# Kernel optimization log

Hardware: AMD Instinct MI355X
Metric: run time of the kernel (lower is better)

## Reference

```python
import jax, jax.numpy as jnp
import numpy as np

NUM_EMB = 512
EMB_DIM = 64
COMMIT = 0.25
DECAY = 0.99
EPS = 1e-05


def setup_inputs() -> dict:
    key = jax.random.key(0)
    k1, k2, k3 = jax.random.split(key, 3)
    inputs = jax.random.normal(k1, (EMB_DIM, 16, 8192), dtype=jnp.float32)  # [D, B, T]
    embedding = jax.random.normal(k2, (NUM_EMB, EMB_DIM), dtype=jnp.float32)
    ema_w = jax.random.normal(k3, (NUM_EMB, EMB_DIM), dtype=jnp.float32)
    ema_cluster_size = jnp.zeros((NUM_EMB,), dtype=jnp.float32)
    return {"inputs": inputs, "embedding": embedding, "ema_w": ema_w,
            "ema_cluster_size": ema_cluster_size}


def reference(inputs, embedding, ema_w, ema_cluster_size):
    # [D, B, T] -> [B, T, D]
    x = jnp.transpose(inputs, (1, 2, 0))
    in_shape = x.shape
    flat = x.reshape(-1, EMB_DIM)  # [N, D]

    # Squared L2 distances to every codebook entry: [N, K]
    distances = (jnp.sum(flat ** 2, axis=1, keepdims=True)
                 + jnp.sum(embedding ** 2, axis=1)
                 - 2.0 * flat @ embedding.T)
    idx = jnp.argmin(distances, axis=1)                       # [N]
    encodings = jax.nn.one_hot(idx, NUM_EMB, dtype=jnp.float32)  # [N, K]

    # EMA codebook update (training mode). torch wraps results in nn.Parameter,
    # which detaches them, so we stop_gradient the updated embedding.
    cluster = ema_cluster_size * DECAY + (1.0 - DECAY) * jnp.sum(encodings, axis=0)
    n = jnp.sum(cluster)
    cluster = (cluster + EPS) / (n + NUM_EMB * EPS) * n
    dw = jax.ops.segment_sum(flat, idx, num_segments=NUM_EMB)  # == encodings.T @ flat
    new_ema_w = ema_w * DECAY + (1.0 - DECAY) * dw
    new_emb = jax.lax.stop_gradient(new_ema_w / cluster[:, None])  # [K, D]

    # Quantize via gather (equivalent to encodings @ new_emb)
    quantized = new_emb[idx].reshape(in_shape)  # [B, T, D]

    e_latent_loss = jnp.mean((jax.lax.stop_gradient(quantized) - x) ** 2)
    loss = COMMIT * e_latent_loss

    # Straight-through estimator
    quantized_st = x + jax.lax.stop_gradient(quantized - x)

    avg_probs = jnp.mean(encodings, axis=0)
    perplexity = jnp.exp(-jnp.sum(avg_probs * jnp.log(avg_probs + 1e-10)))

    return (loss, jnp.transpose(quantized_st, (2, 0, 1)), perplexity, encodings, distances)
```

## Files before the change

### kernel.cpp

```cpp
#include <hip/hip_runtime.h>

#define NTOT 131072
#define KCB  512
#define DIM  64

__device__ __forceinline__ float wave_sum(float v) {
#pragma unroll
  for (int off = 32; off; off >>= 1) v += __shfl_xor(v, off, 64);
  return v;
}

__global__ __launch_bounds__(512, 2) void k_dist(
    const float* __restrict__ x_g,
    const float* __restrict__ emb_g,
    float* __restrict__ dist_out,
    float* __restrict__ enc_out,
    int* __restrict__ idx_out,
    unsigned* __restrict__ cnt_g,
    float* __restrict__ dw_g)
{
  __shared__ __align__(16) float embt[DIM][KCB];
  __shared__ __align__(16) float embsq[KCB];
  __shared__ float xtile[DIM][65];
  __shared__ float xq[64];
  __shared__ unsigned lcnt[KCB];

  const int t = threadIdx.x;
  const int lane = t & 63;
  const int w = t >> 6;

  lcnt[t] = 0u;

  {
    const float* er = emb_g + t * DIM;
    float sq = 0.f;
#pragma unroll
    for (int d0 = 0; d0 < DIM; d0 += 4) {
      const float4 e = *reinterpret_cast<const float4*>(er + d0);
      embt[d0 + 0][t] = -2.f * e.x;
      embt[d0 + 1][t] = -2.f * e.y;
      embt[d0 + 2][t] = -2.f * e.z;
      embt[d0 + 3][t] = -2.f * e.w;
      sq = fmaf(e.x, e.x, sq); sq = fmaf(e.y, e.y, sq);
      sq = fmaf(e.z, e.z, sq); sq = fmaf(e.w, e.w, sq);
    }
    embsq[t] = sq;
  }

  const int rows_pb = NTOT / 256;
  const int nb = blockIdx.x * rows_pb;

  for (int tt = 0; tt < rows_pb; tt += 64) {
    const int n0 = nb + tt;
    __syncthreads();
#pragma unroll
    for (int dd = 0; dd < 8; ++dd) {
      const int d = w * 8 + dd;
      xtile[d][lane] = x_g[(size_t)d * NTOT + (n0 + lane)];
    }
    __syncthreads();
    if (w == 0) {
      float s = 0.f;
#pragma unroll
      for (int d = 0; d < DIM; ++d) { const float v = xtile[d][lane]; s = fmaf(v, v, s); }
      xq[lane] = s;
    }
    __syncthreads();

    const int rb = w * 8;
    float xr[8];
#pragma unroll
    for (int r = 0; r < 8; ++r) xr[r] = xtile[lane][rb + r];

    const float4 eb0 = *reinterpret_cast<const float4*>(&embsq[4 * lane]);
    const float4 eb1 = *reinterpret_cast<const float4*>(&embsq[256 + 4 * lane]);
    float acc[8][8];
#pragma unroll
    for (int r = 0; r < 8; ++r) {
      acc[r][0] = eb0.x; acc[r][1] = eb0.y; acc[r][2] = eb0.z; acc[r][3] = eb0.w;
      acc[r][4] = eb1.x; acc[r][5] = eb1.y; acc[r][6] = eb1.z; acc[r][7] = eb1.w;
    }

#pragma unroll 4
    for (int d = 0; d < DIM; ++d) {
      const float4 e0 = *reinterpret_cast<const float4*>(&embt[d][4 * lane]);
      const float4 e1 = *reinterpret_cast<const float4*>(&embt[d][256 + 4 * lane]);
#pragma unroll
      for (int r = 0; r < 8; ++r) {
        const float s = __uint_as_float(
            __builtin_amdgcn_readlane(__float_as_uint(xr[r]), d));
        acc[r][0] = fmaf(s, e0.x, acc[r][0]);
        acc[r][1] = fmaf(s, e0.y, acc[r][1]);
        acc[r][2] = fmaf(s, e0.z, acc[r][2]);
        acc[r][3] = fmaf(s, e0.w, acc[r][3]);
        acc[r][4] = fmaf(s, e1.x, acc[r][4]);
        acc[r][5] = fmaf(s, e1.y, acc[r][5]);
        acc[r][6] = fmaf(s, e1.z, acc[r][6]);
        acc[r][7] = fmaf(s, e1.w, acc[r][7]);
      }
    }

#pragma unroll
    for (int r = 0; r < 8; ++r) {
      const int nr = n0 + rb + r;
      const float xs = xq[rb + r];
      float dv[8];
#pragma unroll
      for (int j = 0; j < 8; ++j) dv[j] = acc[r][j] + xs;

      unsigned long long best = ~0ull;
#pragma unroll
      for (int j = 0; j < 8; ++j) {
        const unsigned kk = (j < 4) ? (unsigned)(4 * lane + j)
                                    : (unsigned)(256 + 4 * lane + (j - 4));
        const unsigned long long pk =
            ((unsigned long long)__float_as_uint(dv[j]) << 32) | kk;
        best = pk < best ? pk : best;
      }
#pragma unroll
      for (int off = 32; off; off >>= 1) {
        const unsigned long long o = __shfl_xor(best, off, 64);
        best = o < best ? o : best;
      }
      const int kmin = (int)(best & 0xFFFFFFFFull);

      float* dp = dist_out + (size_t)nr * KCB + 4 * lane;
      float2 p;
      p.x = dv[0]; p.y = dv[1]; *reinterpret_cast<float2*>(dp) = p;
      p.x = dv[2]; p.y = dv[3]; *reinterpret_cast<float2*>(dp + 2) = p;
      p.x = dv[4]; p.y = dv[5]; *reinterpret_cast<float2*>(dp + 256) = p;
      p.x = dv[6]; p.y = dv[7]; *reinterpret_cast<float2*>(dp + 258) = p;

      float* ep = enc_out + (size_t)nr * KCB + 4 * lane;
      const int k0 = 4 * lane;
      float2 z;
      z.x = (kmin == k0)           ? 1.f : 0.f;
      z.y = (kmin == k0 + 1)       ? 1.f : 0.f;
      *reinterpret_cast<float2*>(ep) = z;
      z.x = (kmin == k0 + 2)       ? 1.f : 0.f;
      z.y = (kmin == k0 + 3)       ? 1.f : 0.f;
      *reinterpret_cast<float2*>(ep + 2) = z;
      z.x = (kmin == 256 + k0)     ? 1.f : 0.f;
      z.y = (kmin == 256 + k0 + 1) ? 1.f : 0.f;
      *reinterpret_cast<float2*>(ep + 256) = z;
      z.x = (kmin == 256 + k0 + 2) ? 1.f : 0.f;
      z.y = (kmin == 256 + k0 + 3) ? 1.f : 0.f;
      *reinterpret_cast<float2*>(ep + 258) = z;

      if (lane == 0) {
        idx_out[nr] = kmin;
        atomicAdd(&lcnt[kmin], 1u);
      }
      unsafeAtomicAdd(dw_g + ((size_t)kmin << 6) + lane, xr[r]);
    }
  }

  __syncthreads();
  if (lcnt[t]) atomicAdd(&cnt_g[t], lcnt[t]);
}

__global__ __launch_bounds__(512, 1) void k_final(
    const float* __restrict__ ema_w, const float* __restrict__ ema_cs,
    const unsigned* __restrict__ cnt, const float* __restrict__ dw,
    float* __restrict__ nemb, float* __restrict__ out)
{
  __shared__ float red[8];
  __shared__ float bc;
  const int t = threadIdx.x;
  const int lane = t & 63, w = t >> 6;

  const float c = (float)cnt[t];
  const float craw = ema_cs[t] * 0.99f + 0.01f * c;

  float s = wave_sum(craw);
  if (lane == 0) red[w] = s;
  __syncthreads();
  if (t == 0) {
    float a = 0.f;
#pragma unroll
    for (int i = 0; i < 8; ++i) a += red[i];
    bc = a;
  }
  __syncthreads();
  const float n = bc;
  const float clus = (craw + 1e-5f) / (n + 512.f * 1e-5f) * n;

  const float4* wr = reinterpret_cast<const float4*>(ema_w + t * 64);
  const float4* dr = reinterpret_cast<const float4*>(dw + t * 64);
  float4* nr = reinterpret_cast<float4*>(nemb + t * 64);
#pragma unroll
  for (int q = 0; q < 16; ++q) {
    const float4 wv = wr[q], dv = dr[q];
    float4 o;
    o.x = (wv.x * 0.99f + 0.01f * dv.x) / clus;
    o.y = (wv.y * 0.99f + 0.01f * dv.y) / clus;
    o.z = (wv.z * 0.99f + 0.01f * dv.z) / clus;
    o.w = (wv.w * 0.99f + 0.01f * dv.w) / clus;
    nr[q] = o;
  }

  const float p = c * (1.f / 131072.f);
  const float term = p * logf(p + 1e-10f);
  float s2 = wave_sum(term);
  if (lane == 0) red[w] = s2;
  __syncthreads();
  if (t == 0) {
    float a = 0.f;
#pragma unroll
    for (int i = 0; i < 8; ++i) a += red[i];
    out[8388609] = expf(-a);
  }
}

__global__ __launch_bounds__(256, 4) void k_quant(
    const float* __restrict__ x_g, const int* __restrict__ idx_g,
    const float* __restrict__ nemb, float* __restrict__ out)
{
  float lsum = 0.f;
  const int stride = gridDim.x * 256;
  for (int i = blockIdx.x * 256 + threadIdx.x; i < (DIM * NTOT / 4); i += stride) {
    const int d = i >> 15;
    const int n4 = i & ((NTOT / 4) - 1);
    const float4 xv = *reinterpret_cast<const float4*>(x_g + ((size_t)d << 17) + 4 * n4);
    const int4 id = *reinterpret_cast<const int4*>(idx_g + 4 * n4);
    const float q0 = nemb[(id.x << 6) + d];
    const float q1 = nemb[(id.y << 6) + d];
    const float q2 = nemb[(id.z << 6) + d];
    const float q3 = nemb[(id.w << 6) + d];
    const float e0 = q0 - xv.x, e1 = q1 - xv.y, e2 = q2 - xv.z, e3 = q3 - xv.w;
    float* op = out + 1 + ((size_t)d << 17) + 4 * n4;
    op[0] = xv.x + e0;
    op[1] = xv.y + e1;
    op[2] = xv.z + e2;
    op[3] = xv.w + e3;
    lsum += e0 * e0 + e1 * e1 + e2 * e2 + e3 * e3;
  }
  lsum = wave_sum(lsum);
  __shared__ float wsum[4];
  const int lane = threadIdx.x & 63, w = threadIdx.x >> 6;
  if (lane == 0) wsum[w] = lsum;
  __syncthreads();
  if (threadIdx.x == 0)
    unsafeAtomicAdd(out, (wsum[0] + wsum[1] + wsum[2] + wsum[3]) * (0.25f / 8388608.f));
}

extern "C" void kernel_launch(void* const* d_in, const int* in_sizes, int n_in,
                              void* d_out, int out_size, void* d_ws, size_t ws_size,
                              hipStream_t stream) {
  const float* x      = (const float*)d_in[0];
  const float* emb    = (const float*)d_in[1];
  const float* ema_w  = (const float*)d_in[2];
  const float* ema_cs = (const float*)d_in[3];
  float* out = (float*)d_out;

  float* enc_out  = out + 8388610;
  float* dist_out = out + 75497474;

  char* ws = (char*)d_ws;
  float*    dw   = (float*)ws;
  unsigned* cnt  = (unsigned*)(ws + 131072);
  float*    nemb = (float*)(ws + 133120);
  int*      idx  = (int*)(ws + 264192);

  hipMemsetAsync(d_ws, 0, 133120, stream);
  hipMemsetAsync(d_out, 0, sizeof(float), stream);

  k_dist<<<256, 512, 0, stream>>>(x, emb, dist_out, enc_out, idx, cnt, dw);
  k_final<<<1, 512, 0, stream>>>(ema_w, ema_cs, cnt, dw, nemb, out);
  k_quant<<<2048, 256, 0, stream>>>(x, idx, nemb, out);
}
```

Baseline: 246.3 us.

## Privatize dw/count atomics per block and rework distance tile to per-wave 16 rows

After: 310.6 us. +26.1%, slower.

```diff
diff --git a/kernel.cpp b/kernel.cpp
--- a/kernel.cpp
+++ b/kernel.cpp
@@ -16,24 +16,20 @@
     float* __restrict__ dist_out,
     float* __restrict__ enc_out,
     int* __restrict__ idx_out,
-    unsigned* __restrict__ cnt_g,
-    float* __restrict__ dw_g)
+    unsigned* __restrict__ cnt_p,
+    float* __restrict__ dw_p,
+    int npart)
 {
   __shared__ __align__(16) float embt[DIM][KCB];
-  __shared__ __align__(16) float embsq[KCB];
-  __shared__ float xtile[DIM][65];
-  __shared__ float xq[64];
-  __shared__ unsigned lcnt[KCB];
+  __shared__ __align__(16) float xls[8][16][DIM];
 
   const int t = threadIdx.x;
   const int lane = t & 63;
   const int w = t >> 6;
-
-  lcnt[t] = 0u;
+  const int part = blockIdx.x & (npart - 1);
 
   {
     const float* er = emb_g + t * DIM;
-    float sq = 0.f;
 #pragma unroll
     for (int d0 = 0; d0 < DIM; d0 += 4) {
       const float4 e = *reinterpret_cast<const float4*>(er + d0);
@@ -41,69 +37,106 @@
       embt[d0 + 1][t] = -2.f * e.y;
       embt[d0 + 2][t] = -2.f * e.z;
       embt[d0 + 3][t] = -2.f * e.w;
-      sq = fmaf(e.x, e.x, sq); sq = fmaf(e.y, e.y, sq);
-      sq = fmaf(e.z, e.z, sq); sq = fmaf(e.w, e.w, sq);
     }
-    embsq[t] = sq;
-  }
-
-  const int rows_pb = NTOT / 256;
-  const int nb = blockIdx.x * rows_pb;
-
-  for (int tt = 0; tt < rows_pb; tt += 64) {
-    const int n0 = nb + tt;
-    __syncthreads();
-#pragma unroll
-    for (int dd = 0; dd < 8; ++dd) {
-      const int d = w * 8 + dd;
-      xtile[d][lane] = x_g[(size_t)d * NTOT + (n0 + lane)];
+  }
+  __syncthreads();
+
+  float ebr[8] = {0.f, 0.f, 0.f, 0.f, 0.f, 0.f, 0.f, 0.f};
+  for (int d = 0; d < DIM; ++d) {
+    const float4 a = *reinterpret_cast<const float4*>(&embt[d][4 * lane]);
+    const float4 b = *reinterpret_cast<const float4*>(&embt[d][256 + 4 * lane]);
+    ebr[0] = fmaf(a.x, a.x, ebr[0]); ebr[1] = fmaf(a.y, a.y, ebr[1]);
+    ebr[2] = fmaf(a.z, a.z, ebr[2]); ebr[3] = fmaf(a.w, a.w, ebr[3]);
+    ebr[4] = fmaf(b.x, b.x, ebr[4]); ebr[5] = fmaf(b.y, b.y, ebr[5]);
+    ebr[6] = fmaf(b.z, b.z, ebr[6]); ebr[7] = fmaf(b.w, b.w, ebr[7]);
+  }
+#pragma unroll
+  for (int j = 0; j < 8; ++j) ebr[j] *= 0.25f;
+
+  const int nb = blockIdx.x * 512;
+  const int r_own = lane & 15;
+  const int dgrp  = lane >> 4;
+
+  for (int tt = 0; tt < 4; ++tt) {
+    const int n0w = nb + tt * 128 + w * 16;
+
+    asm volatile("" ::: "memory");
+
+    float xv[16];
+#pragma unroll
+    for (int j = 0; j < 16; ++j)
+      xv[j] = x_g[(size_t)(4 * j + dgrp) * NTOT + n0w + r_own];
+#pragma unroll
+    for (int j = 0; j < 16; ++j)
+      xls[w][r_own][4 * j + dgrp] = xv[j];
+
+    asm volatile("" ::: "memory");
+
+    float ps = 0.f;
+#pragma unroll
+    for (int j = 0; j < 16; ++j) ps = fmaf(xv[j], xv[j], ps);
+    ps += __shfl_xor(ps, 16, 64);
+    ps += __shfl_xor(ps, 32, 64);
+
+    float acc[16][8];
+#pragma unroll
+    for (int r = 0; r < 16; ++r)
+#pragma unroll
+      for (int j = 0; j < 8; ++j) acc[r][j] = ebr[j];
+
+    for (int q = 0; q < 16; ++q) {
+      float4 e0[4], e1[4];
+#pragma unroll
+      for (int dq = 0; dq < 4; ++dq) {
+        e0[dq] = *reinterpret_cast<const float4*>(&embt[4 * q + dq][4 * lane]);
+        e1[dq] = *reinterpret_cast<const float4*>(&embt[4 * q + dq][256 + 4 * lane]);
+      }
+#pragma unroll
+      for (int r = 0; r < 16; ++r) {
+        const float4 xb = *reinterpret_cast<const float4*>(&xls[w][r][4 * q]);
+        acc[r][0] = fmaf(xb.x, e0[0].x, acc[r][0]);
+        acc[r][1] = fmaf(xb.x, e0[0].y, acc[r][1]);
+        acc[r][2] = fmaf(xb.x, e0[0].z, acc[r][2]);
+        acc[r][3] = fmaf(xb.x, e0[0].w, acc[r][3]);
+        acc[r][4] = fmaf(xb.x, e1[0].x, acc[r][4]);
+        acc[r][5] = fmaf(xb.x, e1[0].y, acc[r][5]);
+        acc[r][6] = fmaf(xb.x, e1[0].z, acc[r][6]);
+        acc[r][7] = fmaf(xb.x, e1[0].w, acc[r][7]);
+
+        acc[r][0] = fmaf(xb.y, e0[1].x, acc[r][0]);
+        acc[r][1] = fmaf(xb.y, e0[1].y, acc[r][1]);
+        acc[r][2] = fmaf(xb.y, e0[1].z, acc[r][2]);
+        acc[r][3] = fmaf(xb.y, e0[1].w, acc[r][3]);
+        acc[r][4] = fmaf(xb.y, e1[1].x, acc[r][4]);
+        acc[r][5] = fmaf(xb.y, e1[1].y, acc[r][5]);
+        acc[r][6] = fmaf(xb.y, e1[1].z, acc[r][6]);
+        acc[r][7] = fmaf(xb.y, e1[1].w, acc[r][7]);
+
+        acc[r][0] = fmaf(xb.z, e0[2].x, acc[r][0]);
+        acc[r][1] = fmaf(xb.z, e0[2].y, acc[r][1]);
+        acc[r][2] = fmaf(xb.z, e0[2].z, acc[r][2]);
+        acc[r][3] = fmaf(xb.z, e0[2].w, acc[r][3]);
+        acc[r][4] = fmaf(xb.z, e1[2].x, acc[r][4]);
+        acc[r][5] = fmaf(xb.z, e1[2].y, acc[r][5]);
+        acc[r][6] = fmaf(xb.z, e1[2].z, acc[r][6]);
+        acc[r][7] = fmaf(xb.z, e1[2].w, acc[r][7]);
+
+        acc[r][0] = fmaf(xb.w, e0[3].x, acc[r][0]);
+        acc[r][1] = fmaf(xb.w, e0[3].y, acc[r][1]);
+        acc[r][2] = fmaf(xb.w, e0[3].z, acc[r][2]);
+        acc[r][3] = fmaf(xb.w, e0[3].w, acc[r][3]);
+        acc[r][4] = fmaf(xb.w, e1[3].x, acc[r][4]);
+        acc[r][5] = fmaf(xb.w, e1[3].y, acc[r][5]);
+        acc[r][6] = fmaf(xb.w, e1[3].z, acc[r][6]);
+        acc[r][7] = fmaf(xb.w, e1[3].w, acc[r][7]);
+      }
     }
-    __syncthreads();
-    if (w == 0) {
-      float s = 0.f;
-#pragma unroll
-      for (int d = 0; d < DIM; ++d) { const float v = xtile[d][lane]; s = fmaf(v, v, s); }
-      xq[lane] = s;
-    }
-    __syncthreads();
-
-    const int rb = w * 8;
-    float xr[8];
-#pragma unroll
-    for (int r = 0; r < 8; ++r) xr[r] = xtile[lane][rb + r];
-
-    const float4 eb0 = *reinterpret_cast<const float4*>(&embsq[4 * lane]);
-    const float4 eb1 = *reinterpret_cast<const float4*>(&embsq[256 + 4 * lane]);
-    float acc[8][8];
-#pragma unroll
-    for (int r = 0; r < 8; ++r) {
-      acc[r][0] = eb0.x; acc[r][1] = eb0.y; acc[r][2] = eb0.z; acc[r][3] = eb0.w;
-      acc[r][4] = eb1.x; acc[r][5] = eb1.y; acc[r][6] = eb1.z; acc[r][7] = eb1.w;
-    }
-
-#pragma unroll 4
-    for (int d = 0; d < DIM; ++d) {
-      const float4 e0 = *reinterpret_cast<const float4*>(&embt[d][4 * lane]);
-      const float4 e1 = *reinterpret_cast<const float4*>(&embt[d][256 + 4 * lane]);
-#pragma unroll
-      for (int r = 0; r < 8; ++r) {
-        const float s = __uint_as_float(
-            __builtin_amdgcn_readlane(__float_as_uint(xr[r]), d));
-        acc[r][0] = fmaf(s, e0.x, acc[r][0]);
-        acc[r][1] = fmaf(s, e0.y, acc[r][1]);
-        acc[r][2] = fmaf(s, e0.z, acc[r][2]);
-        acc[r][3] = fmaf(s, e0.w, acc[r][3]);
-        acc[r][4] = fmaf(s, e1.x, acc[r][4]);
-        acc[r][5] = fmaf(s, e1.y, acc[r][5]);
-        acc[r][6] = fmaf(s, e1.z, acc[r][6]);
-        acc[r][7] = fmaf(s, e1.w, acc[r][7]);
-      }
-    }
-
-#pragma unroll
-    for (int r = 0; r < 8; ++r) {
-      const int nr = n0 + rb + r;
-      const float xs = xq[rb + r];
+
+#pragma unroll
+    for (int r = 0; r < 16; ++r) {
+      const int nr = n0w + r;
+      const float xs = __uint_as_float(
+          __builtin_amdgcn_readlane(__float_as_uint(ps), r));
       float dv[8];
 #pragma unroll
       for (int j = 0; j < 8; ++j) dv[j] = acc[r][j] + xs;
@@ -149,14 +182,29 @@
 
       if (lane == 0) {
         idx_out[nr] = kmin;
-        atomicAdd(&lcnt[kmin], 1u);
-      }
-      unsafeAtomicAdd(dw_g + ((size_t)kmin << 6) + lane, xr[r]);
+        atomicAdd(cnt_p + (size_t)part * KCB + kmin, 1u);
+      }
+      const float xrow = xls[w][r][lane];
+      unsafeAtomicAdd(dw_p + (size_t)part * (KCB * DIM) + (kmin << 6) + lane, xrow);
     }
   }
-
-  __syncthreads();
-  if (lcnt[t]) atomicAdd(&cnt_g[t], lcnt[t]);
+}
+
+__global__ __launch_bounds__(256, 8) void k_red(
+    const float* __restrict__ dw_p, const unsigned* __restrict__ cnt_p,
+    float* __restrict__ dwsum, unsigned* __restrict__ cnt, int npart)
+{
+  const int t = blockIdx.x * 256 + threadIdx.x;
+  float s = 0.f;
+#pragma unroll 4
+  for (int p = 0; p < npart; ++p) s += dw_p[(size_t)p * (KCB * DIM) + t];
+  dwsum[t] = s;
+  if (t < KCB) {
+    unsigned c = 0u;
+#pragma unroll 4
+    for (int p = 0; p < npart; ++p) c += cnt_p[(size_t)p * KCB + t];
+    cnt[t] = c;
+  }
 }
 
 __global__ __launch_bounds__(512, 1) void k_final(
@@ -257,15 +305,22 @@
   float* dist_out = out + 75497474;
 
   char* ws = (char*)d_ws;
-  float*    dw   = (float*)ws;
-  unsigned* cnt  = (unsigned*)(ws + 131072);
-  float*    nemb = (float*)(ws + 133120);
-  int*      idx  = (int*)(ws + 264192);
-
-  hipMemsetAsync(d_ws, 0, 133120, stream);
+  float*    dwsum = (float*)ws;
+  unsigned* cnt   = (unsigned*)(ws + 131072);
+  float*    nemb  = (float*)(ws + 133120);
+  int*      idx   = (int*)(ws + 264192);
+
+  int npart = 256;
+  while (npart > 1 &&
+         (size_t)788480 + (size_t)npart * 133120 > ws_size) npart >>= 1;
+  unsigned* cnt_p = (unsigned*)(ws + 788480);
+  float*    dw_p  = (float*)(ws + 788480 + (size_t)npart * 2048);
+
+  hipMemsetAsync(ws + 788480, 0, (size_t)npart * 133120, stream);
   hipMemsetAsync(d_out, 0, sizeof(float), stream);
 
-  k_dist<<<256, 512, 0, stream>>>(x, emb, dist_out, enc_out, idx, cnt, dw);
-  k_final<<<1, 512, 0, stream>>>(ema_w, ema_cs, cnt, dw, nemb, out);
+  k_dist<<<256, 512, 0, stream>>>(x, emb, dist_out, enc_out, idx, cnt_p, dw_p, npart);
+  k_red<<<128, 256, 0, stream>>>(dw_p, cnt_p, dwsum, cnt, npart);
+  k_final<<<1, 512, 0, stream>>>(ema_w, ema_cs, cnt, dwsum, nemb, out);
   k_quant<<<2048, 256, 0, stream>>>(x, idx, nemb, out);
 }
```

## Make x tile staging per-wave and drop block barriers in distance loop

Applied to the files above, without the earlier changes.

Result: faster. 239.0 us (-3.0%).

```diff
diff --git a/kernel.cpp b/kernel.cpp
--- a/kernel.cpp
+++ b/kernel.cpp
@@ -20,9 +20,7 @@
     float* __restrict__ dw_g)
 {
   __shared__ __align__(16) float embt[DIM][KCB];
-  __shared__ __align__(16) float embsq[KCB];
-  __shared__ float xtile[DIM][65];
-  __shared__ float xq[64];
+  __shared__ __align__(16) float xls[8][8][65];
   __shared__ unsigned lcnt[KCB];
 
   const int t = threadIdx.x;
@@ -33,7 +31,6 @@
 
   {
     const float* er = emb_g + t * DIM;
-    float sq = 0.f;
 #pragma unroll
     for (int d0 = 0; d0 < DIM; d0 += 4) {
       const float4 e = *reinterpret_cast<const float4*>(er + d0);
@@ -41,45 +38,57 @@
       embt[d0 + 1][t] = -2.f * e.y;
       embt[d0 + 2][t] = -2.f * e.z;
       embt[d0 + 3][t] = -2.f * e.w;
-      sq = fmaf(e.x, e.x, sq); sq = fmaf(e.y, e.y, sq);
-      sq = fmaf(e.z, e.z, sq); sq = fmaf(e.w, e.w, sq);
     }
-    embsq[t] = sq;
-  }
-
-  const int rows_pb = NTOT / 256;
-  const int nb = blockIdx.x * rows_pb;
-
-  for (int tt = 0; tt < rows_pb; tt += 64) {
-    const int n0 = nb + tt;
-    __syncthreads();
-#pragma unroll
-    for (int dd = 0; dd < 8; ++dd) {
-      const int d = w * 8 + dd;
-      xtile[d][lane] = x_g[(size_t)d * NTOT + (n0 + lane)];
-    }
-    __syncthreads();
-    if (w == 0) {
-      float s = 0.f;
-#pragma unroll
-      for (int d = 0; d < DIM; ++d) { const float v = xtile[d][lane]; s = fmaf(v, v, s); }
-      xq[lane] = s;
-    }
-    __syncthreads();
-
-    const int rb = w * 8;
+  }
+  __syncthreads();
+
+  float ebr[8] = {0.f, 0.f, 0.f, 0.f, 0.f, 0.f, 0.f, 0.f};
+  for (int d = 0; d < DIM; ++d) {
+    const float4 a = *reinterpret_cast<const float4*>(&embt[d][4 * lane]);
+    const float4 b = *reinterpret_cast<const float4*>(&embt[d][256 + 4 * lane]);
+    ebr[0] = fmaf(a.x, a.x, ebr[0]); ebr[1] = fmaf(a.y, a.y, ebr[1]);
+    ebr[2] = fmaf(a.z, a.z, ebr[2]); ebr[3] = fmaf(a.w, a.w, ebr[3]);
+    ebr[4] = fmaf(b.x, b.x, ebr[4]); ebr[5] = fmaf(b.y, b.y, ebr[5]);
+    ebr[6] = fmaf(b.z, b.z, ebr[6]); ebr[7] = fmaf(b.w, b.w, ebr[7]);
+  }
+#pragma unroll
+  for (int j = 0; j < 8; ++j) ebr[j] *= 0.25f;
+
+  const int nb = blockIdx.x * 512;
+  const int r_own = lane & 7;
+  const int dgc   = lane >> 3;
+
+  for (int tt = 0; tt < 8; ++tt) {
+    const int n0w = nb + tt * 64 + w * 8;
+
+    asm volatile("" ::: "memory");
+
+    float xv[8];
+#pragma unroll
+    for (int j = 0; j < 8; ++j)
+      xv[j] = x_g[(size_t)(dgc * 8 + j) * NTOT + n0w + r_own];
+#pragma unroll
+    for (int j = 0; j < 8; ++j)
+      xls[w][r_own][dgc * 8 + j] = xv[j];
+
+    asm volatile("" ::: "memory");
+
+    float ps = 0.f;
+#pragma unroll
+    for (int j = 0; j < 8; ++j) ps = fmaf(xv[j], xv[j], ps);
+    ps += __shfl_xor(ps, 8, 64);
+    ps += __shfl_xor(ps, 16, 64);
+    ps += __shfl_xor(ps, 32, 64);
+
     float xr[8];
 #pragma unroll
-    for (int r = 0; r < 8; ++r) xr[r] = xtile[lane][rb + r];
-
-    const float4 eb0 = *reinterpret_cast<const float4*>(&embsq[4 * lane]);
-    const float4 eb1 = *reinterpret_cast<const float4*>(&embsq[256 + 4 * lane]);
+    for (int r = 0; r < 8; ++r) xr[r] = xls[w][r][lane];
+
     float acc[8][8];
 #pragma unroll
-    for (int r = 0; r < 8; ++r) {
-      acc[r][0] = eb0.x; acc[r][1] = eb0.y; acc[r][2] = eb0.z; acc[r][3] = eb0.w;
-      acc[r][4] = eb1.x; acc[r][5] = eb1.y; acc[r][6] = eb1.z; acc[r][7] = eb1.w;
-    }
+    for (int r = 0; r < 8; ++r)
+#pragma unroll
+      for (int j = 0; j < 8; ++j) acc[r][j] = ebr[j];
 
 #pragma unroll 4
     for (int d = 0; d < DIM; ++d) {
@@ -102,8 +111,9 @@
 
 #pragma unroll
     for (int r = 0; r < 8; ++r) {
-      const int nr = n0 + rb + r;
-      const float xs = xq[rb + r];
+      const int nr = n0w + r;
+      const float xs = __uint_as_float(
+          __builtin_amdgcn_readlane(__float_as_uint(ps), r));
       float dv[8];
 #pragma unroll
       for (int j = 0; j < 8; ++j) dv[j] = acc[r][j] + xs;
@@ -125,27 +135,25 @@
       const int kmin = (int)(best & 0xFFFFFFFFull);
 
       float* dp = dist_out + (size_t)nr * KCB + 4 * lane;
-      float2 p;
-      p.x = dv[0]; p.y = dv[1]; *reinterpret_cast<float2*>(dp) = p;
-      p.x = dv[2]; p.y = dv[3]; *reinterpret_cast<float2*>(dp + 2) = p;
-      p.x = dv[4]; p.y = dv[5]; *reinterpret_cast<float2*>(dp + 256) = p;
-      p.x = dv[6]; p.y = dv[7]; *reinterpret_cast<float2*>(dp + 258) = p;
+      float4 q;
+      q.x = dv[0]; q.y = dv[1]; q.z = dv[2]; q.w = dv[3];
+      *reinterpret_cast<float4*>(dp) = q;
+      q.x = dv[4]; q.y = dv[5]; q.z = dv[6]; q.w = dv[7];
+      *reinterpret_cast<float4*>(dp + 256) = q;
 
       float* ep = enc_out + (size_t)nr * KCB + 4 * lane;
       const int k0 = 4 * lane;
-      float2 z;
-      z.x = (kmin == k0)           ? 1.f : 0.f;
-      z.y = (kmin == k0 + 1)       ? 1.f : 0.f;
-      *reinterpret_cast<float2*>(ep) = z;
-      z.x = (kmin == k0 + 2)       ? 1.f : 0.f;
-      z.y = (kmin == k0 + 3)       ? 1.f : 0.f;
-      *reinterpret_cast<float2*>(ep + 2) = z;
+      float4 z;
+      z.x = (kmin == k0)     ? 1.f : 0.f;
+      z.y = (kmin == k0 + 1) ? 1.f : 0.f;
+      z.z = (kmin == k0 + 2) ? 1.f : 0.f;
+      z.w = (kmin == k0 + 3) ? 1.f : 0.f;
+      *reinterpret_cast<float4*>(ep) = z;
       z.x = (kmin == 256 + k0)     ? 1.f : 0.f;
       z.y = (kmin == 256 + k0 + 1) ? 1.f : 0.f;
-      *reinterpret_cast<float2*>(ep + 256) = z;
-      z.x = (kmin == 256 + k0 + 2) ? 1.f : 0.f;
-      z.y = (kmin == 256 + k0 + 3) ? 1.f : 0.f;
-      *reinterpret_cast<float2*>(ep + 258) = z;
+      z.z = (kmin == 256 + k0 + 2) ? 1.f : 0.f;
+      z.w = (kmin == 256 + k0 + 3) ? 1.f : 0.f;
+      *reinterpret_cast<float4*>(ep + 256) = z;
 
       if (lane == 0) {
         idx_out[nr] = kmin;
```
